# Performance work log

Measured on AMD Instinct MI355X. Metric: run time of the kernel, lower is better.

## Reference

```python
import jax, jax.numpy as jnp
import numpy as np

N_NODES = 100000
N_EDGES = 600000
IN_DIM, HID, OUT = 6, 128, 1
EPS = 1e-5


def _glorot(key, shape):
    fan_in, fan_out = shape[1], shape[0]
    lim = jnp.sqrt(6.0 / (fan_in + fan_out))
    return jax.random.uniform(key, shape, jnp.float32, -lim, lim)


def setup_inputs() -> dict:
    key = jax.random.key(0)
    ks = jax.random.split(key, 16)
    x = jax.random.normal(ks[0], (N_NODES, IN_DIM), jnp.float32)
    edge_index = jax.random.randint(ks[1], (2, N_EDGES), 0, N_NODES, jnp.int64)
    return {
        "x": x,
        "edge_index": edge_index,
        # SAGEConv layer 0: 6 -> 128 (lin_l acts on aggregated neighbors, lin_r on root)
        "w_l0": _glorot(ks[2], (HID, IN_DIM)), "b_l0": jnp.zeros((HID,), jnp.float32),
        "w_r0": _glorot(ks[3], (HID, IN_DIM)),
        "bn_g0": jnp.ones((HID,), jnp.float32), "bn_b0": jnp.zeros((HID,), jnp.float32),
        # SAGEConv layer 1: 128 -> 128
        "w_l1": _glorot(ks[4], (HID, HID)), "b_l1": jnp.zeros((HID,), jnp.float32),
        "w_r1": _glorot(ks[5], (HID, HID)),
        "bn_g1": jnp.ones((HID,), jnp.float32), "bn_b1": jnp.zeros((HID,), jnp.float32),
        # SAGEConv layer 2: 128 -> 1
        "w_l2": _glorot(ks[6], (OUT, HID)), "b_l2": jnp.zeros((OUT,), jnp.float32),
        "w_r2": _glorot(ks[7], (OUT, HID)),
    }


def _sage_conv(x, src, dst, inv_deg, w_l, b_l, w_r):
    # mean aggregation of source-node features into destination nodes
    agg = jax.ops.segment_sum(x[src], dst, num_segments=N_NODES)  # [N, d]
    mean_nb = agg * inv_deg[:, None]
    return mean_nb @ w_l.T + b_l + x @ w_r.T


def _batch_norm(x, gamma, beta):
    mu = jnp.mean(x, axis=0)
    var = jnp.mean(jnp.square(x - mu), axis=0)  # biased, as torch BN training
    return (x - mu) * jax.lax.rsqrt(var + EPS) * gamma + beta


def reference(x, edge_index, w_l0, b_l0, w_r0, bn_g0, bn_b0,
              w_l1, b_l1, w_r1, bn_g1, bn_b1, w_l2, b_l2, w_r2):
    src, dst = edge_index[0], edge_index[1]
    deg = jax.ops.segment_sum(jnp.ones_like(dst, dtype=x.dtype), dst,
                              num_segments=N_NODES)
    inv_deg = 1.0 / jnp.maximum(deg, 1.0)

    h = _sage_conv(x, src, dst, inv_deg, w_l0, b_l0, w_r0)
    h = jax.nn.relu(_batch_norm(h, bn_g0, bn_b0))  # dropout = identity (eval)

    h = _sage_conv(h, src, dst, inv_deg, w_l1, b_l1, w_r1)
    h = jax.nn.relu(_batch_norm(h, bn_g1, bn_b1))

    h = _sage_conv(h, src, dst, inv_deg, w_l2, b_l2, w_r2)
    return jax.nn.sigmoid(h).squeeze(-1)  # [N]
```

## Files before the change

### kernel.cpp

```cpp
#include <hip/hip_runtime.h>
#include <math.h>

#define HID 128
#define INDIM 6

typedef float4 f4;
typedef __attribute__((ext_vector_type(8))) short short8;
typedef __attribute__((ext_vector_type(4))) float f32x4;

static __device__ inline unsigned short f2bf(float f) {
    union { float f; unsigned int u; } v; v.f = f;
    unsigned int r = v.u + 0x7fffu + ((v.u >> 16) & 1u);
    return (unsigned short)(r >> 16);
}
static __device__ inline float bf2f_lo(unsigned int u) {
    union { unsigned int u; float f; } v; v.u = u << 16; return v.f;
}
static __device__ inline float bf2f_hi(unsigned int u) {
    union { unsigned int u; float f; } v; v.u = u & 0xffff0000u; return v.f;
}

__global__ void k_zero2(int* a, int na, int* b, int nb) {
    int i = blockIdx.x * blockDim.x + threadIdx.x;
    if (i < na) a[i] = 0;
    if (i < nb) b[i] = 0;
}

__global__ void k_deg(const int* dst, int* deg, int* rank, int E) {
    int e = blockIdx.x * blockDim.x + threadIdx.x;
    if (e < E) rank[e] = atomicAdd(&deg[dst[e]], 1);
}

__global__ void k_scan_partial(const int* __restrict__ deg, int* __restrict__ partial, int N) {
    __shared__ int lds[256];
    int t = threadIdx.x;
    int base = blockIdx.x * 1024 + t * 4;
    int s = 0;
    if (base + 4 <= N) {
        int4 v = *(const int4*)&deg[base];
        s = v.x + v.y + v.z + v.w;
    } else {
        for (int i = 0; i < 4; i++) if (base + i < N) s += deg[base + i];
    }
    lds[t] = s;
    __syncthreads();
    for (int off = 128; off > 0; off >>= 1) {
        if (t < off) lds[t] += lds[t + off];
        __syncthreads();
    }
    if (t == 0) partial[blockIdx.x] = lds[0];
}

__global__ void k_scan_tops(int* partial, int nb) {
    __shared__ int lds[1024];
    int t = threadIdx.x;
    lds[t] = (t < nb) ? partial[t] : 0;
    __syncthreads();
    for (int off = 1; off < 1024; off <<= 1) {
        int v = (t >= off) ? lds[t - off] : 0;
        __syncthreads();
        lds[t] += v;
        __syncthreads();
    }
    if (t < nb) partial[t] = (t == 0) ? 0 : lds[t - 1];
}

__global__ void k_scan_write(const int* __restrict__ deg, const int* __restrict__ partial,
                             int* __restrict__ rowptr, float* __restrict__ invd,
                             int N, int E) {
    __shared__ int lds[256];
    int t = threadIdx.x;
    int base = blockIdx.x * 1024 + t * 4;
    int v0 = 0, v1 = 0, v2 = 0, v3 = 0;
    if (base + 4 <= N) {
        int4 v = *(const int4*)&deg[base];
        v0 = v.x; v1 = v.y; v2 = v.z; v3 = v.w;
    } else {
        if (base + 0 < N) v0 = deg[base + 0];
        if (base + 1 < N) v1 = deg[base + 1];
        if (base + 2 < N) v2 = deg[base + 2];
        if (base + 3 < N) v3 = deg[base + 3];
    }
    lds[t] = v0 + v1 + v2 + v3;
    __syncthreads();
    for (int off = 1; off < 256; off <<= 1) {
        int v = (t >= off) ? lds[t - off] : 0;
        __syncthreads();
        lds[t] += v;
        __syncthreads();
    }
    int run = partial[blockIdx.x] + ((t == 0) ? 0 : lds[t - 1]);
    if (base + 0 < N) { rowptr[base + 0] = run; invd[base + 0] = 1.0f / (float)max(v0, 1); } run += v0;
    if (base + 1 < N) { rowptr[base + 1] = run; invd[base + 1] = 1.0f / (float)max(v1, 1); } run += v1;
    if (base + 2 < N) { rowptr[base + 2] = run; invd[base + 2] = 1.0f / (float)max(v2, 1); } run += v2;
    if (base + 3 < N) { rowptr[base + 3] = run; invd[base + 3] = 1.0f / (float)max(v3, 1); } run += v3;
    if (blockIdx.x == 0 && t == 0) rowptr[N] = E;
}

__global__ void k_fill(const int* ei, const int* rank, const int* rowptr, int* csr, int E) {
    int e = blockIdx.x * blockDim.x + threadIdx.x;
    if (e < E) {
        int d = ei[E + e];
        csr[rowptr[d] + rank[e]] = ei[e];
    }
}

__global__ void k_prepw(const float* __restrict__ wl, const float* __restrict__ wr,
                        unsigned short* __restrict__ wcat) {
    int i = blockIdx.x * 256 + threadIdx.x;
    int o = i >> 8, k = i & 255;
    float v = (k < 128) ? wl[o * 128 + k] : wr[o * 128 + k - 128];
    wcat[i] = f2bf(v);
}

__global__ __launch_bounds__(256) void k_l0stats(
        const float* __restrict__ x, const int* __restrict__ rowptr,
        const int* __restrict__ csr, const float* __restrict__ invd,
        const float* __restrict__ wl, const float* __restrict__ bl,
        const float* __restrict__ wr, float* __restrict__ mean6,
        float* __restrict__ sum8, float* __restrict__ sq8, int N) {
    __shared__ float wlds[1600];
    __shared__ float blds[136];
    __shared__ float mx[32][8];
    __shared__ float xr[32][8];
    __shared__ float ps[4][128];
    __shared__ float pq[4][128];
    int t = threadIdx.x;
    for (int idx = t; idx < 1536; idx += 256) {
        int half = idx >= 768 ? 1 : 0;
        int lin = idx - half * 768;
        int o = lin / 6, i = lin - o * 6;
        float v = half ? wr[lin] : wl[lin];
        wlds[half * 800 + o * 6 + i + (o >> 4) * 2] = v;
    }
    if (t < 128) blds[t + (t >> 4)] = bl[t];
    int nl = t >> 3, f = t & 7;
    int n = blockIdx.x * 32 + nl;
    bool valid = n < N;
    if (f < 6) {
        float mean = 0.f, xv = 0.f;
        if (valid) {
            int s = rowptr[n], e = rowptr[n + 1];
            float acc = 0.f;
            int i = s;
            for (; i + 4 <= e; i += 4) {
                int i0 = csr[i], i1 = csr[i + 1], i2 = csr[i + 2], i3 = csr[i + 3];
                float a0 = x[i0 * 6 + f], a1 = x[i1 * 6 + f];
                float a2 = x[i2 * 6 + f], a3 = x[i3 * 6 + f];
                acc += (a0 + a1) + (a2 + a3);
            }
            for (; i < e; i++) acc += x[csr[i] * 6 + f];
            mean = acc * invd[n];
            xv = x[n * 6 + f];
            mean6[n * 6 + f] = mean;
        }
        mx[nl][f] = mean;
        xr[nl][f] = xv;
    }
    __syncthreads();
    float m0 = mx[nl][0], m1 = mx[nl][1], m2 = mx[nl][2];
    float m3 = mx[nl][3], m4 = mx[nl][4], m5 = mx[nl][5];
    float r0 = xr[nl][0], r1 = xr[nl][1], r2 = xr[nl][2];
    float r3 = xr[nl][3], r4 = xr[nl][4], r5 = xr[nl][5];
    const float* wA = wlds;
    const float* wB = wlds + 800;
    int wv = t >> 6, lane = t & 63;
#pragma unroll
    for (int k = 0; k < 16; k++) {
        int o = f * 16 + k;
        int wb = 98 * f + 6 * k;
        float h = blds[o + f];
        h += m0 * wA[wb] + m1 * wA[wb + 1] + m2 * wA[wb + 2]
           + m3 * wA[wb + 3] + m4 * wA[wb + 4] + m5 * wA[wb + 5];
        h += r0 * wB[wb] + r1 * wB[wb + 1] + r2 * wB[wb + 2]
           + r3 * wB[wb + 3] + r4 * wB[wb + 4] + r5 * wB[wb + 5];
        float s = valid ? h : 0.f;
        float q = s * s;
        s += __shfl_xor(s, 8, 64);  q += __shfl_xor(q, 8, 64);
        s += __shfl_xor(s, 16, 64); q += __shfl_xor(q, 16, 64);
        s += __shfl_xor(s, 32, 64); q += __shfl_xor(q, 32, 64);
        if (lane < 8) { ps[wv][lane * 16 + k] = s; pq[wv][lane * 16 + k] = q; }
    }
    __syncthreads();
    if (t < 128) {
        float S = ps[0][t] + ps[1][t] + ps[2][t] + ps[3][t];
        float Q = pq[0][t] + pq[1][t] + pq[2][t] + pq[3][t];
        int slot = (blockIdx.x & 7) * 128 + t;
        atomicAdd(&sum8[slot], S);
        atomicAdd(&sq8[slot], Q);
    }
}

__global__ __launch_bounds__(256) void k_l0apply(
        const float* __restrict__ x, const float* __restrict__ mean6,
        const float* __restrict__ wl, const float* __restrict__ bl,
        const float* __restrict__ wr, const float* __restrict__ scale,
        const float* __restrict__ shift, unsigned short* __restrict__ out, int N) {
    __shared__ float wlds[1600];
    __shared__ float blds[136];
    __shared__ float sclds[136];
    __shared__ float shlds[136];
    __shared__ float mx[32][8];
    __shared__ float xr[32][8];
    int t = threadIdx.x;
    for (int idx = t; idx < 1536; idx += 256) {
        int half = idx >= 768 ? 1 : 0;
        int lin = idx - half * 768;
        int o = lin / 6, i = lin - o * 6;
        float v = half ? wr[lin] : wl[lin];
        wlds[half * 800 + o * 6 + i + (o >> 4) * 2] = v;
    }
    if (t < 128) {
        blds[t + (t >> 4)]  = bl[t];
        sclds[t + (t >> 4)] = scale[t];
        shlds[t + (t >> 4)] = shift[t];
    }
    int nl = t >> 3, f = t & 7;
    int n = blockIdx.x * 32 + nl;
    bool valid = n < N;
    if (f < 6) {
        mx[nl][f] = valid ? mean6[n * 6 + f] : 0.f;
        xr[nl][f] = valid ? x[n * 6 + f] : 0.f;
    }
    __syncthreads();
    if (!valid) return;
    float m0 = mx[nl][0], m1 = mx[nl][1], m2 = mx[nl][2];
    float m3 = mx[nl][3], m4 = mx[nl][4], m5 = mx[nl][5];
    float r0 = xr[nl][0], r1 = xr[nl][1], r2 = xr[nl][2];
    float r3 = xr[nl][3], r4 = xr[nl][4], r5 = xr[nl][5];
    const float* wA = wlds;
    const float* wB = wlds + 800;
    unsigned short pk[16];
#pragma unroll
    for (int k4 = 0; k4 < 4; k4++) {
#pragma unroll
        for (int j = 0; j < 4; j++) {
            int k = k4 * 4 + j;
            int o = f * 16 + k;
            int wb = 98 * f + 6 * k;
            float h = blds[o + f];
            h += m0 * wA[wb] + m1 * wA[wb + 1] + m2 * wA[wb + 2]
               + m3 * wA[wb + 3] + m4 * wA[wb + 4] + m5 * wA[wb + 5];
            h += r0 * wB[wb] + r1 * wB[wb + 1] + r2 * wB[wb + 2]
               + r3 * wB[wb + 3] + r4 * wB[wb + 4] + r5 * wB[wb + 5];
            pk[k] = f2bf(fmaxf(0.f, fmaf(h, sclds[o + f], shlds[o + f])));
        }
    }
    unsigned short* dst = out + (size_t)n * HID + f * 16;
    *(uint4*)(dst)     = *(const uint4*)&pk[0];
    *(uint4*)(dst + 8) = *(const uint4*)&pk[8];
}

__global__ void k_bnfin8(const float* sum8, const float* sq8, const float* g, const float* b,
                         float* scale, float* shift, float invN) {
    int t = threadIdx.x;
    float s = 0.f, q = 0.f;
    for (int c = 0; c < 8; c++) { s += sum8[c * 128 + t]; q += sq8[c * 128 + t]; }
    float mu  = s * invN;
    float var = q * invN - mu * mu;
    float sc  = g[t] * rsqrtf(var + 1e-5f);
    scale[t] = sc;
    shift[t] = b[t] - mu * sc;
}

__global__ void k_agg_bf(const unsigned short* __restrict__ hb, const int* __restrict__ rowptr,
                         const int* __restrict__ csr, const float* __restrict__ invd,
                         unsigned short* __restrict__ out, int N) {
    int t = threadIdx.x;
    int w = t >> 6, lid = t & 63;
    int q = lid >> 4, l16 = lid & 15;
    int n = blockIdx.x * 16 + w * 4 + q;
    if (n >= N) return;
    int s = rowptr[n], e = rowptr[n + 1];
    const uint4* hb128 = (const uint4*)hb;
    float ax0 = 0.f, ay0 = 0.f, ax1 = 0.f, ay1 = 0.f;
    float ax2 = 0.f, ay2 = 0.f, ax3 = 0.f, ay3 = 0.f;
    int i = s;
    for (; i + 4 <= e; i += 4) {
        int i0 = csr[i], i1 = csr[i + 1], i2 = csr[i + 2], i3 = csr[i + 3];
        uint4 u0 = hb128[(size_t)i0 * 16 + l16];
        uint4 u1 = hb128[(size_t)i1 * 16 + l16];
        uint4 u2 = hb128[(size_t)i2 * 16 + l16];
        uint4 u3 = hb128[(size_t)i3 * 16 + l16];
        ax0 += (bf2f_lo(u0.x) + bf2f_lo(u1.x)) + (bf2f_lo(u2.x) + bf2f_lo(u3.x));
        ay0 += (bf2f_hi(u0.x) + bf2f_hi(u1.x)) + (bf2f_hi(u2.x) + bf2f_hi(u3.x));
        ax1 += (bf2f_lo(u0.y) + bf2f_lo(u1.y)) + (bf2f_lo(u2.y) + bf2f_lo(u3.y));
        ay1 += (bf2f_hi(u0.y) + bf2f_hi(u1.y)) + (bf2f_hi(u2.y) + bf2f_hi(u3.y));
        ax2 += (bf2f_lo(u0.z) + bf2f_lo(u1.z)) + (bf2f_lo(u2.z) + bf2f_lo(u3.z));
        ay2 += (bf2f_hi(u0.z) + bf2f_hi(u1.z)) + (bf2f_hi(u2.z) + bf2f_hi(u3.z));
        ax3 += (bf2f_lo(u0.w) + bf2f_lo(u1.w)) + (bf2f_lo(u2.w) + bf2f_lo(u3.w));
        ay3 += (bf2f_hi(u0.w) + bf2f_hi(u1.w)) + (bf2f_hi(u2.w) + bf2f_hi(u3.w));
    }
    for (; i < e; i++) {
        uint4 u = hb128[(size_t)csr[i] * 16 + l16];
        ax0 += bf2f_lo(u.x); ay0 += bf2f_hi(u.x);
        ax1 += bf2f_lo(u.y); ay1 += bf2f_hi(u.y);
        ax2 += bf2f_lo(u.z); ay2 += bf2f_hi(u.z);
        ax3 += bf2f_lo(u.w); ay3 += bf2f_hi(u.w);
    }
    float id = invd[n];
    uint4 r;
    r.x = (unsigned int)f2bf(ax0 * id) | ((unsigned int)f2bf(ay0 * id) << 16);
    r.y = (unsigned int)f2bf(ax1 * id) | ((unsigned int)f2bf(ay1 * id) << 16);
    r.z = (unsigned int)f2bf(ax2 * id) | ((unsigned int)f2bf(ay2 * id) << 16);
    r.w = (unsigned int)f2bf(ax3 * id) | ((unsigned int)f2bf(ay3 * id) << 16);
    ((uint4*)out)[(size_t)n * 16 + l16] = r;
}

__global__ __launch_bounds__(256) void k_gemm(
        const unsigned short* __restrict__ Bm, const unsigned short* __restrict__ Ar,
        const unsigned short* __restrict__ wcat, const float* __restrict__ bias,
        float* __restrict__ sum8, float* __restrict__ sq8,
        unsigned short* __restrict__ C, int N) {
    __shared__ __align__(16) unsigned short As[128][72];
    __shared__ __align__(16) unsigned short Ws[128][72];
    __shared__ float lds_s[2][128];
    __shared__ float lds_q[2][128];
    int t = threadIdx.x;
    int wave = t >> 6, lane = t & 63;
    int wr = wave >> 1, wc = wave & 1;
    int row0 = blockIdx.x * 128;
    int r = t >> 1, half = t & 1;
    int lrow = lane & 15, koff = (lane >> 4) * 8;

    f32x4 acc[4][4];
#pragma unroll
    for (int m = 0; m < 4; m++)
#pragma unroll
        for (int n = 0; n < 4; n++) acc[m][n] = (f32x4)(0.f);

    for (int chunk = 0; chunk < 4; chunk++) {
        int kb = chunk * 64;
        int srow = row0 + r;
        int c0 = (kb & 127) + half * 32;
        const unsigned short* src = (kb < 128) ? Bm : Ar;
        uint4 a0, a1, a2, a3;
        if (srow < N) {
            const unsigned short* p = src + (size_t)srow * HID + c0;
            a0 = *(const uint4*)(p);      a1 = *(const uint4*)(p + 8);
            a2 = *(const uint4*)(p + 16); a3 = *(const uint4*)(p + 24);
        } else {
            a0 = a1 = a2 = a3 = make_uint4(0, 0, 0, 0);
        }
        *(uint4*)&As[r][half * 32]      = a0;
        *(uint4*)&As[r][half * 32 + 8]  = a1;
        *(uint4*)&As[r][half * 32 + 16] = a2;
        *(uint4*)&As[r][half * 32 + 24] = a3;
        const unsigned short* wp = wcat + r * 256 + kb + half * 32;
        *(uint4*)&Ws[r][half * 32]      = *(const uint4*)(wp);
        *(uint4*)&Ws[r][half * 32 + 8]  = *(const uint4*)(wp + 8);
        *(uint4*)&Ws[r][half * 32 + 16] = *(const uint4*)(wp + 16);
        *(uint4*)&Ws[r][half * 32 + 24] = *(const uint4*)(wp + 24);
        __syncthreads();

#pragma unroll
        for (int ks = 0; ks < 64; ks += 32) {
            short8 af[4], bfr[4];
#pragma unroll
            for (int m = 0; m < 4; m++)
                af[m] = *(const short8*)&As[wr * 64 + m * 16 + lrow][ks + koff];
#pragma unroll
            for (int n = 0; n < 4; n++)
                bfr[n] = *(const short8*)&Ws[wc * 64 + n * 16 + lrow][ks + koff];
#pragma unroll
            for (int m = 0; m < 4; m++)
#pragma unroll
                for (int n = 0; n < 4; n++)
                    acc[m][n] = __builtin_amdgcn_mfma_f32_16x16x32_bf16(af[m], bfr[n], acc[m][n], 0, 0, 0);
        }
        __syncthreads();
    }

    unsigned short* Cst = &As[0][0];
    int cl = lane & 15, rq = (lane >> 4) * 4;
    float cs[4], cq[4];
#pragma unroll
    for (int n = 0; n < 4; n++) {
        int col = wc * 64 + n * 16 + cl;
        float bn = bias[col];
        float s = 0.f, q = 0.f;
#pragma unroll
        for (int m = 0; m < 4; m++) {
#pragma unroll
            for (int reg = 0; reg < 4; reg++) {
                int rl = wr * 64 + m * 16 + rq + reg;
                float v = acc[m][n][reg] + bn;
                Cst[rl * 136 + col] = f2bf(v);
                if (row0 + rl < N) { s += v; q += v * v; }
            }
        }
        cs[n] = s; cq[n] = q;
    }
#pragma unroll
    for (int n = 0; n < 4; n++) {
        float s = cs[n], q = cq[n];
        s += __shfl_xor(s, 16, 64); q += __shfl_xor(q, 16, 64);
        s += __shfl_xor(s, 32, 64); q += __shfl_xor(q, 32, 64);
        if (lane < 16) {
            int col = wc * 64 + n * 16 + cl;
            lds_s[wr][col] = s;
            lds_q[wr][col] = q;
        }
    }
    __syncthreads();
    if (t < 128) {
        float S = lds_s[0][t] + lds_s[1][t];
        float Q = lds_q[0][t] + lds_q[1][t];
        int slot = (blockIdx.x & 7) * 128 + t;
        atomicAdd(&sum8[slot], S);
        atomicAdd(&sq8[slot], Q);
    }
#pragma unroll
    for (int j = 0; j < 8; j++) {
        int idx = t + j * 256;
        int rl = idx >> 4, seg = idx & 15;
        int row = row0 + rl;
        if (row < N)
            *(uint4*)(C + (size_t)row * HID + seg * 8) = *(const uint4*)&Cst[rl * 136 + seg * 8];
    }
}

__global__ void k_dots(const unsigned short* __restrict__ h, const float* __restrict__ scale,
                       const float* __restrict__ shift, const float* __restrict__ wl2,
                       const float* __restrict__ wr2, float* __restrict__ s_arr,
                       float* __restrict__ r_arr, int N) {
    int w = threadIdx.x >> 6, lid = threadIdx.x & 63;
    int n = blockIdx.x * 4 + w;
    if (n >= N) return;
    unsigned int u = ((const unsigned int*)h)[(size_t)n * 64 + lid];
    float hx = bf2f_lo(u), hy = bf2f_hi(u);
    float2 sc = *(const float2*)&scale[lid * 2];
    float2 sh = *(const float2*)&shift[lid * 2];
    float y0 = fmaxf(0.f, fmaf(hx, sc.x, sh.x));
    float y1 = fmaxf(0.f, fmaf(hy, sc.y, sh.y));
    float2 wl = *(const float2*)&wl2[lid * 2];
    float2 wrv = *(const float2*)&wr2[lid * 2];
    float ps = y0 * wl.x + y1 * wl.y;
    float pr = y0 * wrv.x + y1 * wrv.y;
#pragma unroll
    for (int off = 32; off > 0; off >>= 1) {
        ps += __shfl_down(ps, off, 64);
        pr += __shfl_down(pr, off, 64);
    }
    if (lid == 0) { s_arr[n] = ps; r_arr[n] = pr; }
}

__global__ void k_final2(const float* __restrict__ s_arr, const float* __restrict__ r_arr,
                         const int* __restrict__ rowptr, const int* __restrict__ csr,
                         const float* __restrict__ invd, const float* __restrict__ bl2,
                         float* __restrict__ out, int N) {
    int n = blockIdx.x * blockDim.x + threadIdx.x;
    if (n >= N) return;
    int s = rowptr[n], e = rowptr[n + 1];
    float a = 0.f;
    int i = s;
    for (; i + 4 <= e; i += 4) {
        float a0 = s_arr[csr[i]],     a1 = s_arr[csr[i + 1]];
        float a2 = s_arr[csr[i + 2]], a3 = s_arr[csr[i + 3]];
        a += (a0 + a1) + (a2 + a3);
    }
    for (; i < e; i++) a += s_arr[csr[i]];
    float p = a * invd[n] + r_arr[n] + bl2[0];
    out[n] = 1.f / (1.f + expf(-p));
}

extern "C" void kernel_launch(void* const* d_in, const int* in_sizes, int n_in,
                              void* d_out, int out_size, void* d_ws, size_t ws_size,
                              hipStream_t stream) {
    const float* x   = (const float*)d_in[0];
    const int*   ei  = (const int*)d_in[1];
    const float* wl0 = (const float*)d_in[2];
    const float* bl0 = (const float*)d_in[3];
    const float* wr0 = (const float*)d_in[4];
    const float* g0  = (const float*)d_in[5];
    const float* be0 = (const float*)d_in[6];
    const float* wl1 = (const float*)d_in[7];
    const float* bl1 = (const float*)d_in[8];
    const float* wr1 = (const float*)d_in[9];
    const float* g1  = (const float*)d_in[10];
    const float* be1 = (const float*)d_in[11];
    const float* wl2 = (const float*)d_in[12];
    const float* bl2 = (const float*)d_in[13];
    const float* wr2 = (const float*)d_in[14];
    float* outp = (float*)d_out;

    int N = in_sizes[0] / INDIM;
    int E = in_sizes[1] / 2;

    char* ws = (char*)d_ws;
    size_t off = 0;
    auto alloc = [&](size_t bytes) { size_t o = off; off = (off + bytes + 255) & ~(size_t)255; return o; };
    int*   degi   = (int*)(ws + alloc((size_t)N * 4));
    int*   rank   = (int*)(ws + alloc((size_t)E * 4));
    int*   rowptr = (int*)(ws + alloc((size_t)(N + 1) * 4));
    int*   csr    = (int*)(ws + alloc((size_t)E * 4));
    float* invd   = (float*)(ws + alloc((size_t)N * 4));
    int*   partial= (int*)(ws + alloc(1024 * 4));
    float* bnbuf  = (float*)(ws + alloc(5120 * 4));
    unsigned short* wcat = (unsigned short*)(ws + alloc(128 * 256 * 2));
    float* sarr   = (float*)(ws + alloc((size_t)N * 4));
    float* rarr   = (float*)(ws + alloc((size_t)N * 4));
    float* mean6  = (float*)(ws + alloc((size_t)N * 6 * 4));
    float* sum0_8 = bnbuf;
    float* sq0_8  = bnbuf + 1024;
    float* sum1_8 = bnbuf + 2048;
    float* sq1_8  = bnbuf + 3072;
    float* sc0 = bnbuf + 4096, *sh0 = bnbuf + 4224;
    float* sc1 = bnbuf + 4352, *sh1 = bnbuf + 4480;
    unsigned short* bufB = (unsigned short*)(ws + alloc((size_t)N * HID * 2));
    unsigned short* bufC = (unsigned short*)(ws + alloc((size_t)N * HID * 2));
    unsigned short* bufD = (unsigned short*)(ws + alloc((size_t)N * HID * 2));

    float invN = 1.0f / (float)N;
    int gE = (E + 255) / 256;
    int gN = (N + 255) / 256;
    int gW = (N + 3) / 4;
    int gA = (N + 15) / 16;
    int gL = (N + 31) / 32;
    int gS = (N + 127) / 128;
    int nbScan = (N + 1023) / 1024;

    k_zero2<<<gN, 256, 0, stream>>>(degi, N, (int*)bnbuf, 4096);

    k_prepw<<<128, 256, 0, stream>>>(wl1, wr1, wcat);

    k_deg<<<gE, 256, 0, stream>>>(ei + E, degi, rank, E);
    k_scan_partial<<<nbScan, 256, 0, stream>>>(degi, partial, N);
    k_scan_tops<<<1, 1024, 0, stream>>>(partial, nbScan);
    k_scan_write<<<nbScan, 256, 0, stream>>>(degi, partial, rowptr, invd, N, E);
    k_fill<<<gE, 256, 0, stream>>>(ei, rank, rowptr, csr, E);

    k_l0stats<<<gL, 256, 0, stream>>>(x, rowptr, csr, invd, wl0, bl0, wr0, mean6,
                                      sum0_8, sq0_8, N);
    k_bnfin8<<<1, 128, 0, stream>>>(sum0_8, sq0_8, g0, be0, sc0, sh0, invN);

    k_l0apply<<<gL, 256, 0, stream>>>(x, mean6, wl0, bl0, wr0, sc0, sh0, bufC, N);

    k_agg_bf<<<gA, 256, 0, stream>>>(bufC, rowptr, csr, invd, bufD, N);
    k_gemm<<<gS, 256, 0, stream>>>(bufD, bufC, wcat, bl1, sum1_8, sq1_8, bufB, N);
    k_bnfin8<<<1, 128, 0, stream>>>(sum1_8, sq1_8, g1, be1, sc1, sh1, invN);

    k_dots<<<gW, 256, 0, stream>>>(bufB, sc1, sh1, wl2, wr2, sarr, rarr, N);
    k_final2<<<gN, 256, 0, stream>>>(sarr, rarr, rowptr, csr, invd, bl2, outp, N);
}
```

Baseline: 187.4 us.

## Halve GEMM row tile to 64 and fuse weight prep into init kernel

The layer-1 GEMM now uses 64-row tiles, with each of the four waves computing a 64x32 output slice instead of a 2x2 wave grid over 128x128. This doubles the block count for better CU occupancy and load balance, shrinks the accumulator registers, and reuses the weight LDS buffer for output staging. In exchange, weight tiles are reloaded twice as often per row. Separately, the weight bf16 conversion is merged into the zeroing kernel, removing one launch.

```diff
diff --git a/kernel.cpp b/kernel.cpp
--- a/kernel.cpp
+++ b/kernel.cpp
@@ -20,10 +20,17 @@
     union { unsigned int u; float f; } v; v.u = u & 0xffff0000u; return v.f;
 }
 
-__global__ void k_zero2(int* a, int na, int* b, int nb) {
+__global__ void k_init(int* a, int na, int* b, int nb,
+                       const float* __restrict__ wl, const float* __restrict__ wr,
+                       unsigned short* __restrict__ wcat) {
     int i = blockIdx.x * blockDim.x + threadIdx.x;
     if (i < na) a[i] = 0;
     if (i < nb) b[i] = 0;
+    if (i < 32768) {
+        int o = i >> 8, k = i & 255;
+        float v = (k < 128) ? wl[o * 128 + k] : wr[o * 128 + k - 128];
+        wcat[i] = f2bf(v);
+    }
 }
 
 __global__ void k_deg(const int* dst, int* deg, int* rank, int E) {
@@ -103,14 +110,6 @@
         int d = ei[E + e];
         csr[rowptr[d] + rank[e]] = ei[e];
     }
-}
-
-__global__ void k_prepw(const float* __restrict__ wl, const float* __restrict__ wr,
-                        unsigned short* __restrict__ wcat) {
-    int i = blockIdx.x * 256 + threadIdx.x;
-    int o = i >> 8, k = i & 255;
-    float v = (k < 128) ? wl[o * 128 + k] : wr[o * 128 + k - 128];
-    wcat[i] = f2bf(v);
 }
 
 __global__ __launch_bounds__(256) void k_l0stats(
@@ -312,106 +311,91 @@
         const unsigned short* __restrict__ wcat, const float* __restrict__ bias,
         float* __restrict__ sum8, float* __restrict__ sq8,
         unsigned short* __restrict__ C, int N) {
-    __shared__ __align__(16) unsigned short As[128][72];
+    __shared__ __align__(16) unsigned short As[64][72];
     __shared__ __align__(16) unsigned short Ws[128][72];
-    __shared__ float lds_s[2][128];
-    __shared__ float lds_q[2][128];
+    __shared__ float lds_s[128];
+    __shared__ float lds_q[128];
     int t = threadIdx.x;
     int wave = t >> 6, lane = t & 63;
-    int wr = wave >> 1, wc = wave & 1;
-    int row0 = blockIdx.x * 128;
-    int r = t >> 1, half = t & 1;
+    int row0 = blockIdx.x * 64;
     int lrow = lane & 15, koff = (lane >> 4) * 8;
 
-    f32x4 acc[4][4];
+    f32x4 acc[4][2];
 #pragma unroll
     for (int m = 0; m < 4; m++)
 #pragma unroll
-        for (int n = 0; n < 4; n++) acc[m][n] = (f32x4)(0.f);
+        for (int n = 0; n < 2; n++) acc[m][n] = (f32x4)(0.f);
 
     for (int chunk = 0; chunk < 4; chunk++) {
         int kb = chunk * 64;
-        int srow = row0 + r;
-        int c0 = (kb & 127) + half * 32;
+        int rA = t >> 2, qA = t & 3;
+        int srow = row0 + rA;
+        int cA = (kb & 127) + qA * 16;
         const unsigned short* src = (kb < 128) ? Bm : Ar;
-        uint4 a0, a1, a2, a3;
+        uint4 a0, a1;
         if (srow < N) {
-            const unsigned short* p = src + (size_t)srow * HID + c0;
-            a0 = *(const uint4*)(p);      a1 = *(const uint4*)(p + 8);
-            a2 = *(const uint4*)(p + 16); a3 = *(const uint4*)(p + 24);
+            const unsigned short* p = src + (size_t)srow * HID + cA;
+            a0 = *(const uint4*)(p); a1 = *(const uint4*)(p + 8);
         } else {
-            a0 = a1 = a2 = a3 = make_uint4(0, 0, 0, 0);
+            a0 = a1 = make_uint4(0, 0, 0, 0);
         }
-        *(uint4*)&As[r][half * 32]      = a0;
-        *(uint4*)&As[r][half * 32 + 8]  = a1;
-        *(uint4*)&As[r][half * 32 + 16] = a2;
-        *(uint4*)&As[r][half * 32 + 24] = a3;
-        const unsigned short* wp = wcat + r * 256 + kb + half * 32;
-        *(uint4*)&Ws[r][half * 32]      = *(const uint4*)(wp);
-        *(uint4*)&Ws[r][half * 32 + 8]  = *(const uint4*)(wp + 8);
-        *(uint4*)&Ws[r][half * 32 + 16] = *(const uint4*)(wp + 16);
-        *(uint4*)&Ws[r][half * 32 + 24] = *(const uint4*)(wp + 24);
+        *(uint4*)&As[rA][qA * 16]     = a0;
+        *(uint4*)&As[rA][qA * 16 + 8] = a1;
+        int rW = t >> 1, hW = t & 1;
+        const unsigned short* wp = wcat + rW * 256 + kb + hW * 32;
+        *(uint4*)&Ws[rW][hW * 32]      = *(const uint4*)(wp);
+        *(uint4*)&Ws[rW][hW * 32 + 8]  = *(const uint4*)(wp + 8);
+        *(uint4*)&Ws[rW][hW * 32 + 16] = *(const uint4*)(wp + 16);
+        *(uint4*)&Ws[rW][hW * 32 + 24] = *(const uint4*)(wp + 24);
         __syncthreads();
 
 #pragma unroll
         for (int ks = 0; ks < 64; ks += 32) {
-            short8 af[4], bfr[4];
+            short8 af[4], bfr[2];
 #pragma unroll
             for (int m = 0; m < 4; m++)
-                af[m] = *(const short8*)&As[wr * 64 + m * 16 + lrow][ks + koff];
-#pragma unroll
-            for (int n = 0; n < 4; n++)
-                bfr[n] = *(const short8*)&Ws[wc * 64 + n * 16 + lrow][ks + koff];
+                af[m] = *(const short8*)&As[m * 16 + lrow][ks + koff];
+#pragma unroll
+            for (int n = 0; n < 2; n++)
+                bfr[n] = *(const short8*)&Ws[wave * 32 + n * 16 + lrow][ks + koff];
 #pragma unroll
             for (int m = 0; m < 4; m++)
 #pragma unroll
-                for (int n = 0; n < 4; n++)
+                for (int n = 0; n < 2; n++)
                     acc[m][n] = __builtin_amdgcn_mfma_f32_16x16x32_bf16(af[m], bfr[n], acc[m][n], 0, 0, 0);
         }
         __syncthreads();
     }
 
-    unsigned short* Cst = &As[0][0];
+    unsigned short* Cst = &Ws[0][0];
     int cl = lane & 15, rq = (lane >> 4) * 4;
-    float cs[4], cq[4];
-#pragma unroll
-    for (int n = 0; n < 4; n++) {
-        int col = wc * 64 + n * 16 + cl;
+#pragma unroll
+    for (int n = 0; n < 2; n++) {
+        int col = wave * 32 + n * 16 + cl;
         float bn = bias[col];
         float s = 0.f, q = 0.f;
 #pragma unroll
         for (int m = 0; m < 4; m++) {
 #pragma unroll
             for (int reg = 0; reg < 4; reg++) {
-                int rl = wr * 64 + m * 16 + rq + reg;
+                int rl = m * 16 + rq + reg;
                 float v = acc[m][n][reg] + bn;
                 Cst[rl * 136 + col] = f2bf(v);
                 if (row0 + rl < N) { s += v; q += v * v; }
             }
         }
-        cs[n] = s; cq[n] = q;
-    }
-#pragma unroll
-    for (int n = 0; n < 4; n++) {
-        float s = cs[n], q = cq[n];
         s += __shfl_xor(s, 16, 64); q += __shfl_xor(q, 16, 64);
         s += __shfl_xor(s, 32, 64); q += __shfl_xor(q, 32, 64);
-        if (lane < 16) {
-            int col = wc * 64 + n * 16 + cl;
-            lds_s[wr][col] = s;
-            lds_q[wr][col] = q;
-        }
+        if (lane < 16) { lds_s[col] = s; lds_q[col] = q; }
     }
     __syncthreads();
     if (t < 128) {
-        float S = lds_s[0][t] + lds_s[1][t];
-        float Q = lds_q[0][t] + lds_q[1][t];
         int slot = (blockIdx.x & 7) * 128 + t;
-        atomicAdd(&sum8[slot], S);
-        atomicAdd(&sq8[slot], Q);
-    }
-#pragma unroll
-    for (int j = 0; j < 8; j++) {
+        atomicAdd(&sum8[slot], lds_s[t]);
+        atomicAdd(&sq8[slot], lds_q[t]);
+    }
+#pragma unroll
+    for (int j = 0; j < 4; j++) {
         int idx = t + j * 256;
         int rl = idx >> 4, seg = idx & 15;
         int row = row0 + rl;
@@ -517,12 +501,10 @@
     int gW = (N + 3) / 4;
     int gA = (N + 15) / 16;
     int gL = (N + 31) / 32;
-    int gS = (N + 127) / 128;
+    int gS = (N + 63) / 64;
     int nbScan = (N + 1023) / 1024;
 
-    k_zero2<<<gN, 256, 0, stream>>>(degi, N, (int*)bnbuf, 4096);
-
-    k_prepw<<<128, 256, 0, stream>>>(wl1, wr1, wcat);
+    k_init<<<gN, 256, 0, stream>>>(degi, N, (int*)bnbuf, 4096, wl1, wr1, wcat);
 
     k_deg<<<gE, 256, 0, stream>>>(ei + E, degi, rank, E);
     k_scan_partial<<<nbScan, 256, 0, stream>>>(degi, partial, N);
```

Result: faster. 182.2 us (-2.8%).
